# Kernel tuning notes

Hardware: AMD Instinct MI355X
Metric: run time of the kernel (lower is better)

Reference implementation:

```python
import jax, jax.numpy as jnp
import numpy as np

N = 8192
E = 131072
C_IN = 256
C_OUT = 256


def setup_inputs() -> dict:
    key = jax.random.key(0)
    k1, k2, k3, k4 = jax.random.split(key, 4)
    x = jax.random.normal(k1, (N, C_IN), dtype=jnp.float32)
    edge_index = jax.random.randint(k2, (2, E), 0, N, dtype=jnp.int64)
    # nn.Linear params (PyTorch layout: W is (out, in))
    bound = 1.0 / np.sqrt(C_IN)
    W = jax.random.uniform(k3, (C_OUT, C_IN), minval=-bound, maxval=bound, dtype=jnp.float32)
    b_lin = jax.random.uniform(k4, (C_OUT,), minval=-bound, maxval=bound, dtype=jnp.float32)
    bias = jnp.zeros((C_OUT,), dtype=jnp.float32)  # extra learned bias parameter
    return {"x": x, "W": W, "b_lin": b_lin, "bias": bias, "edge_index": edge_index}


def reference(x, W, b_lin, bias, edge_index):
    n = x.shape[0]
    # Dense adjacency built by scatter ASSIGNMENT (duplicate edges collapse to 1.0),
    # matching torch's adj[e0, e1] = 1.0
    adj = jnp.zeros((n, n), dtype=x.dtype).at[edge_index[0], edge_index[1]].set(1.0)
    # adj = adj + eye (diagonal entries can become 2.0 if self-loop edge exists)
    diag = jnp.arange(n)
    adj = adj.at[diag, diag].add(1.0)
    deg = adj.sum(axis=1)
    # pow(deg, -0.5) with inf -> 0 (deg == 0 case)
    deg_inv_sqrt = jnp.where(deg > 0, 1.0 / jnp.sqrt(deg), 0.0)
    # symmetric normalization: D^-1/2 A D^-1/2
    norm = deg_inv_sqrt[:, None] * adj * deg_inv_sqrt[None, :]
    out = norm @ x                      # (N, C_in)
    out = out @ W.T + b_lin + bias      # (N, C_out)
    return out
```

## Files before the change

### kernel.cpp

```cpp
#include <hip/hip_runtime.h>
#include <stdint.h>

#define N_NODES 8192
#define CH      256
#define NWORDS  256
#define BM_BYTES (N_NODES * NWORDS * 4)
#define DEG_CAP 64

typedef short bf16x8 __attribute__((ext_vector_type(8)));
typedef float f32x4  __attribute__((ext_vector_type(4)));

static __device__ __forceinline__ unsigned short f2bf(float f) {
    union { float f; uint32_t u; } v; v.f = f;
    uint32_t r = v.u + 0x7fff + ((v.u >> 16) & 1);
    return (unsigned short)(r >> 16);
}
static __device__ __forceinline__ uint32_t pack2bf(float lo, float hi) {
    return (uint32_t)f2bf(lo) | ((uint32_t)f2bf(hi) << 16);
}
static __device__ __forceinline__ float bfbits_lo(uint32_t u) {
    union { uint32_t u; float f; } v; v.u = u << 16; return v.f;
}
static __device__ __forceinline__ float bfbits_hi(uint32_t u) {
    union { uint32_t u; float f; } v; v.u = u & 0xffff0000u; return v.f;
}

__global__ void k_edges(const int* __restrict__ ei, uint32_t* __restrict__ bm,
                        int* __restrict__ cnt, unsigned short* __restrict__ csr, int E) {
    int e = blockIdx.x * blockDim.x + threadIdx.x;
    if (e >= E) return;
    int r = ei[e];
    int c = ei[E + e];
    uint32_t bit = 1u << (c & 31);
    uint32_t old = atomicOr(&bm[r * NWORDS + (c >> 5)], bit);
    if (!(old & bit)) {
        int p = atomicAdd(&cnt[r], 1);
        if (p < DEG_CAP) csr[r * DEG_CAP + p] = (unsigned short)c;
    }
}

__global__ __launch_bounds__(256) void k_deg_y(const int* __restrict__ cnt,
                                               const float* __restrict__ x,
                                               const float* __restrict__ W,
                                               uint32_t* __restrict__ y,
                                               uint32_t* __restrict__ Wb) {
    int lane = threadIdx.x & 63;
    int wid  = threadIdx.x >> 6;
    if (blockIdx.x < 2048) {
        int row = blockIdx.x * 4 + wid;
        float di = rsqrtf((float)(cnt[row] + 1));
        float4 xv = ((const float4*)(x + (size_t)row * CH))[lane];
        uint2 o;
        o.x = pack2bf(di * xv.x, di * xv.y);
        o.y = pack2bf(di * xv.z, di * xv.w);
        ((uint2*)y)[row * 64 + lane] = o;
    } else {
        int i = (blockIdx.x - 2048) * 1024 + threadIdx.x * 4;
        float4 wv = *(const float4*)(W + i);
        uint2 o;
        o.x = pack2bf(wv.x, wv.y);
        o.y = pack2bf(wv.z, wv.w);
        *(uint2*)(Wb + i / 2) = o;
    }
}

__global__ __launch_bounds__(512) void k_agg_gemm(
    const int* __restrict__ cnt, const unsigned short* __restrict__ csr,
    const uint32_t* __restrict__ y, const unsigned short* __restrict__ Wb,
    const float* __restrict__ b1, const float* __restrict__ b2,
    float* __restrict__ out)
{
    const int tid  = threadIdx.x;
    const int bid  = blockIdx.x;
    const int lane = tid & 63;
    const int wid  = tid >> 6;

    __shared__ uint2 s_o1[16 * 66];

    const uint2* ys = (const uint2*)y;

    #pragma unroll
    for (int rr = 0; rr < 2; ++rr) {
        int rloc = wid * 2 + rr;
        int row  = bid * 16 + rloc;
        int total = cnt[row];
        if (total > DEG_CAP) total = DEG_CAP;
        float di = rsqrtf((float)(total + 1));
        int nb = (lane < total) ? (int)csr[row * DEG_CAP + lane] : 0;

        uint2 d = ys[row * 64 + lane];
        float a0 = bfbits_lo(d.x), a1 = bfbits_hi(d.x);
        float a2 = bfbits_lo(d.y), a3 = bfbits_hi(d.y);
        int k = 0;
        for (; k + 8 <= total; k += 8) {
            int j[8];
            #pragma unroll
            for (int u = 0; u < 8; ++u) j[u] = __shfl(nb, k + u);
            uint2 dv[8];
            #pragma unroll
            for (int u = 0; u < 8; ++u) dv[u] = ys[j[u] * 64 + lane];
            #pragma unroll
            for (int u = 0; u < 8; ++u) {
                a0 += bfbits_lo(dv[u].x); a1 += bfbits_hi(dv[u].x);
                a2 += bfbits_lo(dv[u].y); a3 += bfbits_hi(dv[u].y);
            }
        }
        for (; k < total; ++k) {
            uint2 dd = ys[__shfl(nb, k) * 64 + lane];
            a0 += bfbits_lo(dd.x); a1 += bfbits_hi(dd.x);
            a2 += bfbits_lo(dd.y); a3 += bfbits_hi(dd.y);
        }
        uint2 o;
        o.x = pack2bf(di * a0, di * a1);
        o.y = pack2bf(di * a2, di * a3);
        s_o1[rloc * 66 + lane] = o;
    }
    __syncthreads();

    {
        int m16  = lane & 15;
        int quad = lane >> 4;
        f32x4 acc0 = {0.f, 0.f, 0.f, 0.f};
        f32x4 acc1 = {0.f, 0.f, 0.f, 0.f};
        #pragma unroll
        for (int k0 = 0; k0 < CH; k0 += 32) {
            uint4 av = *(const uint4*)&s_o1[m16 * 66 + (k0 >> 2) + quad * 2];
            bf16x8 af = __builtin_bit_cast(bf16x8, av);
            const unsigned short* w0 = Wb + (size_t)(wid * 32 + m16) * CH + k0 + quad * 8;
            bf16x8 bv0 = *(const bf16x8*)w0;
            acc0 = __builtin_amdgcn_mfma_f32_16x16x32_bf16(af, bv0, acc0, 0, 0, 0);
            bf16x8 bv1 = *(const bf16x8*)(w0 + 16 * CH);
            acc1 = __builtin_amdgcn_mfma_f32_16x16x32_bf16(af, bv1, acc1, 0, 0, 0);
        }
        int rowB = bid * 16 + quad * 4;
        int col0 = wid * 32 + m16;
        float bb0 = b1[col0] + b2[col0];
        float bb1 = b1[col0 + 16] + b2[col0 + 16];
        #pragma unroll
        for (int r = 0; r < 4; ++r)
            out[(size_t)(rowB + r) * CH + col0] = acc0[r] + bb0;
        #pragma unroll
        for (int r = 0; r < 4; ++r)
            out[(size_t)(rowB + r) * CH + col0 + 16] = acc1[r] + bb1;
    }
}

extern "C" void kernel_launch(void* const* d_in, const int* in_sizes, int n_in,
                              void* d_out, int out_size, void* d_ws, size_t ws_size,
                              hipStream_t stream) {
    const float* x   = (const float*)d_in[0];
    const float* W   = (const float*)d_in[1];
    const float* b1  = (const float*)d_in[2];
    const float* b2  = (const float*)d_in[3];
    const int*   ei  = (const int*)d_in[4];
    int E = in_sizes[4] / 2;
    float* out = (float*)d_out;

    uint8_t* ws = (uint8_t*)d_ws;
    uint32_t*       bm  = (uint32_t*)ws;
    int*            cnt = (int*)(ws + BM_BYTES);
    unsigned short* csr = (unsigned short*)(ws + BM_BYTES + 32 * 1024);
    uint32_t*       y   = (uint32_t*)(ws + (12u << 20));
    uint32_t*       Wb  = (uint32_t*)(ws + (16u << 20));

    hipMemsetAsync(bm, 0, BM_BYTES + 32 * 1024, stream);
    k_edges<<<(E + 255) / 256, 256, 0, stream>>>(ei, bm, cnt, csr, E);
    k_deg_y<<<2048 + 64, 256, 0, stream>>>(cnt, x, W, y, Wb);
    k_agg_gemm<<<N_NODES / 16, 512, 0, stream>>>(cnt, csr, y, (const unsigned short*)Wb,
                                                 b1, b2, out);
}
```

Baseline: 101.3 us.

## Drop prescaled bf16 feature pass; gather fp32 x with per-neighbor degree scaling

Removes the intermediate kernel that wrote degree-scaled bf16 features and instead gathers fp32 rows of x directly in the aggregation kernel. Each neighbor's inverse-sqrt degree is looked up and shuffled alongside its index. The W-to-bf16 conversion is folded into the edge kernel, which cuts one launch and one full read-write pass over the features. In exchange, the gather now reads twice as many bytes per neighbor and adds a dependent cnt lookup, and the unroll depth drops from 8 to 4.

New measurement: 104.8 us. +3.5%, slower.

```diff
diff --git a/kernel.cpp b/kernel.cpp
--- a/kernel.cpp
+++ b/kernel.cpp
@@ -6,6 +6,7 @@
 #define NWORDS  256
 #define BM_BYTES (N_NODES * NWORDS * 4)
 #define DEG_CAP 64
+#define EDGE_BLKS 512
 
 typedef short bf16x8 __attribute__((ext_vector_type(8)));
 typedef float f32x4  __attribute__((ext_vector_type(4)));
@@ -18,44 +19,25 @@
 static __device__ __forceinline__ uint32_t pack2bf(float lo, float hi) {
     return (uint32_t)f2bf(lo) | ((uint32_t)f2bf(hi) << 16);
 }
-static __device__ __forceinline__ float bfbits_lo(uint32_t u) {
-    union { uint32_t u; float f; } v; v.u = u << 16; return v.f;
-}
-static __device__ __forceinline__ float bfbits_hi(uint32_t u) {
-    union { uint32_t u; float f; } v; v.u = u & 0xffff0000u; return v.f;
-}
 
-__global__ void k_edges(const int* __restrict__ ei, uint32_t* __restrict__ bm,
-                        int* __restrict__ cnt, unsigned short* __restrict__ csr, int E) {
-    int e = blockIdx.x * blockDim.x + threadIdx.x;
-    if (e >= E) return;
-    int r = ei[e];
-    int c = ei[E + e];
-    uint32_t bit = 1u << (c & 31);
-    uint32_t old = atomicOr(&bm[r * NWORDS + (c >> 5)], bit);
-    if (!(old & bit)) {
-        int p = atomicAdd(&cnt[r], 1);
-        if (p < DEG_CAP) csr[r * DEG_CAP + p] = (unsigned short)c;
-    }
-}
-
-__global__ __launch_bounds__(256) void k_deg_y(const int* __restrict__ cnt,
-                                               const float* __restrict__ x,
-                                               const float* __restrict__ W,
-                                               uint32_t* __restrict__ y,
-                                               uint32_t* __restrict__ Wb) {
-    int lane = threadIdx.x & 63;
-    int wid  = threadIdx.x >> 6;
-    if (blockIdx.x < 2048) {
-        int row = blockIdx.x * 4 + wid;
-        float di = rsqrtf((float)(cnt[row] + 1));
-        float4 xv = ((const float4*)(x + (size_t)row * CH))[lane];
-        uint2 o;
-        o.x = pack2bf(di * xv.x, di * xv.y);
-        o.y = pack2bf(di * xv.z, di * xv.w);
-        ((uint2*)y)[row * 64 + lane] = o;
+__global__ void k_edges_wconv(const int* __restrict__ ei, uint32_t* __restrict__ bm,
+                              int* __restrict__ cnt, unsigned short* __restrict__ csr,
+                              int E, const float* __restrict__ W,
+                              uint32_t* __restrict__ Wb) {
+    int b = blockIdx.x;
+    if (b < EDGE_BLKS) {
+        int e = b * 256 + threadIdx.x;
+        if (e >= E) return;
+        int r = ei[e];
+        int c = ei[E + e];
+        uint32_t bit = 1u << (c & 31);
+        uint32_t old = atomicOr(&bm[r * NWORDS + (c >> 5)], bit);
+        if (!(old & bit)) {
+            int p = atomicAdd(&cnt[r], 1);
+            if (p < DEG_CAP) csr[r * DEG_CAP + p] = (unsigned short)c;
+        }
     } else {
-        int i = (blockIdx.x - 2048) * 1024 + threadIdx.x * 4;
+        int i = (b - EDGE_BLKS) * 1024 + threadIdx.x * 4;
         float4 wv = *(const float4*)(W + i);
         uint2 o;
         o.x = pack2bf(wv.x, wv.y);
@@ -66,7 +48,7 @@
 
 __global__ __launch_bounds__(512) void k_agg_gemm(
     const int* __restrict__ cnt, const unsigned short* __restrict__ csr,
-    const uint32_t* __restrict__ y, const unsigned short* __restrict__ Wb,
+    const float* __restrict__ x, const unsigned short* __restrict__ Wb,
     const float* __restrict__ b1, const float* __restrict__ b2,
     float* __restrict__ out)
 {
@@ -77,7 +59,7 @@
 
     __shared__ uint2 s_o1[16 * 66];
 
-    const uint2* ys = (const uint2*)y;
+    const float4* xs = (const float4*)x;
 
     #pragma unroll
     for (int rr = 0; rr < 2; ++rr) {
@@ -86,29 +68,33 @@
         int total = cnt[row];
         if (total > DEG_CAP) total = DEG_CAP;
         float di = rsqrtf((float)(total + 1));
-        int nb = (lane < total) ? (int)csr[row * DEG_CAP + lane] : 0;
+        int   nb = (lane < total) ? (int)csr[row * DEG_CAP + lane] : 0;
+        int   cj = (lane < total) ? cnt[nb] : 0;
+        float dj = rsqrtf((float)(cj + 1));
 
-        uint2 d = ys[row * 64 + lane];
-        float a0 = bfbits_lo(d.x), a1 = bfbits_hi(d.x);
-        float a2 = bfbits_lo(d.y), a3 = bfbits_hi(d.y);
+        float4 sv = xs[row * 64 + lane];
+        float a0 = di * sv.x, a1 = di * sv.y, a2 = di * sv.z, a3 = di * sv.w;
+
         int k = 0;
-        for (; k + 8 <= total; k += 8) {
-            int j[8];
-            #pragma unroll
-            for (int u = 0; u < 8; ++u) j[u] = __shfl(nb, k + u);
-            uint2 dv[8];
-            #pragma unroll
-            for (int u = 0; u < 8; ++u) dv[u] = ys[j[u] * 64 + lane];
-            #pragma unroll
-            for (int u = 0; u < 8; ++u) {
-                a0 += bfbits_lo(dv[u].x); a1 += bfbits_hi(dv[u].x);
-                a2 += bfbits_lo(dv[u].y); a3 += bfbits_hi(dv[u].y);
-            }
+        for (; k + 4 <= total; k += 4) {
+            int   j0 = __shfl(nb, k),     j1 = __shfl(nb, k + 1);
+            int   j2 = __shfl(nb, k + 2), j3 = __shfl(nb, k + 3);
+            float d0 = __shfl(dj, k),     d1 = __shfl(dj, k + 1);
+            float d2 = __shfl(dj, k + 2), d3 = __shfl(dj, k + 3);
+            float4 v0 = xs[j0 * 64 + lane];
+            float4 v1 = xs[j1 * 64 + lane];
+            float4 v2 = xs[j2 * 64 + lane];
+            float4 v3 = xs[j3 * 64 + lane];
+            a0 += d0 * v0.x; a1 += d0 * v0.y; a2 += d0 * v0.z; a3 += d0 * v0.w;
+            a0 += d1 * v1.x; a1 += d1 * v1.y; a2 += d1 * v1.z; a3 += d1 * v1.w;
+            a0 += d2 * v2.x; a1 += d2 * v2.y; a2 += d2 * v2.z; a3 += d2 * v2.w;
+            a0 += d3 * v3.x; a1 += d3 * v3.y; a2 += d3 * v3.z; a3 += d3 * v3.w;
         }
         for (; k < total; ++k) {
-            uint2 dd = ys[__shfl(nb, k) * 64 + lane];
-            a0 += bfbits_lo(dd.x); a1 += bfbits_hi(dd.x);
-            a2 += bfbits_lo(dd.y); a3 += bfbits_hi(dd.y);
+            int   j = __shfl(nb, k);
+            float d = __shfl(dj, k);
+            float4 v = xs[j * 64 + lane];
+            a0 += d * v.x; a1 += d * v.y; a2 += d * v.z; a3 += d * v.w;
         }
         uint2 o;
         o.x = pack2bf(di * a0, di * a1);
@@ -160,12 +146,10 @@
     uint32_t*       bm  = (uint32_t*)ws;
     int*            cnt = (int*)(ws + BM_BYTES);
     unsigned short* csr = (unsigned short*)(ws + BM_BYTES + 32 * 1024);
-    uint32_t*       y   = (uint32_t*)(ws + (12u << 20));
-    uint32_t*       Wb  = (uint32_t*)(ws + (16u << 20));
+    uint32_t*       Wb  = (uint32_t*)(ws + (10u << 20));
 
     hipMemsetAsync(bm, 0, BM_BYTES + 32 * 1024, stream);
-    k_edges<<<(E + 255) / 256, 256, 0, stream>>>(ei, bm, cnt, csr, E);
-    k_deg_y<<<2048 + 64, 256, 0, stream>>>(cnt, x, W, y, Wb);
-    k_agg_gemm<<<N_NODES / 16, 512, 0, stream>>>(cnt, csr, y, (const unsigned short*)Wb,
+    k_edges_wconv<<<EDGE_BLKS + 64, 256, 0, stream>>>(ei, bm, cnt, csr, E, W, Wb);
+    k_agg_gemm<<<N_NODES / 16, 512, 0, stream>>>(cnt, csr, x, (const unsigned short*)Wb,
                                                  b1, b2, out);
 }
```
